# Kernel optimization log

Measured on AMD Instinct MI355X. Metric: run time of the kernel, lower is better.

The kernel has to match this reference:

```python
import jax, jax.numpy as jnp
import numpy as np

MIN_EXPERT_CAPACITY = 4
EPS = 1e-9
CAPACITY_FACTOR = 2.0  # eval capacity factor


def cumsum_exclusive(t, axis):
    return jnp.cumsum(t, axis=axis) - t


def safe_one_hot(idx, depth):
    # one_hot with an extra slot so idx == depth maps to nothing, then slice
    return jax.nn.one_hot(idx, depth + 1)[..., :depth]


def setup_inputs() -> dict:
    key = jax.random.key(0)
    k_x, k_g, k_w1, k_w2 = jax.random.split(key, 4)
    b, n, d, e, h = 2, 4096, 512, 16, 2048
    x = jax.random.normal(k_x, (b, n, d), dtype=jnp.float32)
    w_gating = jax.random.normal(k_g, (d, e), dtype=jnp.float32) / np.sqrt(d)
    w1 = jax.random.normal(k_w1, (e, d, h), dtype=jnp.float32) / np.sqrt(d)
    w2 = jax.random.normal(k_w2, (e, h, d), dtype=jnp.float32) / np.sqrt(h)
    return {"x": x, "w_gating": w_gating, "w1": w1, "w2": w2}


def top2_gating(x, w_gating):
    b, n, d = x.shape
    e = w_gating.shape[-1]
    raw_gates = jax.nn.softmax(jnp.einsum('bnd,de->bne', x, w_gating), axis=-1)

    gate_1 = jnp.max(raw_gates, axis=-1)
    index_1 = jnp.argmax(raw_gates, axis=-1)
    mask_1 = jax.nn.one_hot(index_1, e, dtype=raw_gates.dtype)

    gates_without_top1 = raw_gates * (1.0 - mask_1)
    gate_2 = jnp.max(gates_without_top1, axis=-1)
    index_2 = jnp.argmax(gates_without_top1, axis=-1)
    mask_2 = jax.nn.one_hot(index_2, e, dtype=raw_gates.dtype)

    denom = gate_1 + gate_2 + EPS
    gate_1 = gate_1 / denom
    gate_2 = gate_2 / denom

    # load-balancing loss
    density_1 = jnp.mean(mask_1, axis=-2)
    density_1_proxy = jnp.mean(raw_gates, axis=-2)
    loss = jnp.mean(density_1_proxy * density_1) * float(e * e)

    # second policy == 'all' -> keep mask_2 as-is

    capacity = max(min(n, int((n * 2) * CAPACITY_FACTOR / e)), MIN_EXPERT_CAPACITY)
    cap_f = float(capacity)

    pos1 = cumsum_exclusive(mask_1, axis=-2) * mask_1  # [b,n,e]
    mask_1 = mask_1 * (pos1 < cap_f).astype(mask_1.dtype)
    mask_1_count = jnp.sum(mask_1, axis=-2, keepdims=True)
    mask_1_flat = jnp.sum(mask_1, axis=-1)  # [b,n]
    pos1 = jnp.sum(pos1, axis=-1)
    gate_1 = gate_1 * mask_1_flat

    pos2 = (cumsum_exclusive(mask_2, axis=-2) + mask_1_count) * mask_2
    mask_2 = mask_2 * (pos2 < cap_f).astype(mask_2.dtype)
    mask_2_flat = jnp.sum(mask_2, axis=-1)
    pos2 = jnp.sum(pos2, axis=-1)
    gate_2 = gate_2 * mask_2_flat

    # combine tensor: [b, n, e, c]
    combine = (gate_1[..., None, None] * mask_1_flat[..., None, None]
               * jax.nn.one_hot(index_1, e, dtype=x.dtype)[..., None]
               * safe_one_hot(pos1.astype(jnp.int32), capacity)[..., None, :]
               + gate_2[..., None, None] * mask_2_flat[..., None, None]
               * jax.nn.one_hot(index_2, e, dtype=x.dtype)[..., None]
               * safe_one_hot(pos2.astype(jnp.int32), capacity)[..., None, :])
    dispatch = (combine > 0).astype(combine.dtype)
    return dispatch, combine, loss


def reference(x, w_gating, w1, w2):
    dispatch, combine, loss = top2_gating(x, w_gating)
    # dispatch: gather tokens into expert buckets [e, b, c, d]
    expert_inputs = jnp.einsum('bnd,bnec->ebcd', x, dispatch)
    # expert FFN (eval mode: dropout is identity)
    hidden = jax.nn.relu(jnp.einsum('ebcd,edh->ebch', expert_inputs, w1))
    expert_outputs = jnp.einsum('ebch,ehd->ebcd', hidden, w2)
    # combine back to token order, weighted by gate values
    output = jnp.einsum('ebcd,bnec->bnd', expert_outputs, combine)
    return output
```

## Files before the change

### kernel.cpp

```cpp
#include <hip/hip_runtime.h>

#define BB 2
#define NN 4096
#define DD 512
#define EE 16
#define HH 2048
#define CAP 1024
#define NTOK (BB*NN)
#define MM (BB*CAP)
#define MAXSTRIP 160

typedef unsigned short ushort_t;
typedef __attribute__((ext_vector_type(8))) short bf16x8;
typedef __attribute__((ext_vector_type(4))) float floatx4;

__device__ __forceinline__ ushort_t f2bf(float f) {
    union { float f; unsigned u; } v; v.f = f;
    unsigned r = v.u + 0x7fffu + ((v.u >> 16) & 1u);
    return (ushort_t)(r >> 16);
}

__device__ __forceinline__ void cp16(const void* g, void* l) {
    __builtin_amdgcn_global_load_lds(
        (const __attribute__((address_space(1))) void*)g,
        (__attribute__((address_space(3))) void*)l, 16, 0, 0);
}

__launch_bounds__(256)
__global__ void gating_kernel(const float* __restrict__ x,
                              const float* __restrict__ wg,
                              int* __restrict__ e1, int* __restrict__ e2,
                              float* __restrict__ g1, float* __restrict__ g2) {
    int wave = threadIdx.x >> 6;
    int lane = threadIdx.x & 63;
    int t = blockIdx.x * 4 + wave;
    const float* xp = x + (size_t)t * DD;

    float acc[EE];
#pragma unroll
    for (int e = 0; e < EE; e++) acc[e] = 0.f;
    for (int d = lane; d < DD; d += 64) {
        float xv = xp[d];
        const float* wrow = wg + d * EE;
#pragma unroll
        for (int e = 0; e < EE; e++) acc[e] = fmaf(xv, wrow[e], acc[e]);
    }
#pragma unroll
    for (int off = 32; off > 0; off >>= 1) {
#pragma unroll
        for (int e = 0; e < EE; e++) acc[e] += __shfl_xor(acc[e], off, 64);
    }
    if (lane == 0) {
        float m = acc[0];
#pragma unroll
        for (int e = 1; e < EE; e++) m = fmaxf(m, acc[e]);
        float p[EE]; float s = 0.f;
#pragma unroll
        for (int e = 0; e < EE; e++) { p[e] = __expf(acc[e] - m); s += p[e]; }
        float inv = 1.f / s;
#pragma unroll
        for (int e = 0; e < EE; e++) p[e] *= inv;
        int i1 = 0; float v1 = p[0];
#pragma unroll
        for (int e = 1; e < EE; e++) if (p[e] > v1) { v1 = p[e]; i1 = e; }
        int i2 = (i1 == 0) ? 1 : 0; float v2 = p[i2];
#pragma unroll
        for (int e = 0; e < EE; e++)
            if (e != i1 && p[e] > v2) { v2 = p[e]; i2 = e; }
        float denom = v1 + v2 + 1e-9f;
        e1[t] = i1; e2[t] = i2;
        g1[t] = v1 / denom; g2[t] = v2 / denom;
    }
}

__launch_bounds__(256)
__global__ void scan_kernel(const int* __restrict__ e1, const int* __restrict__ e2,
                            const float* __restrict__ g1, const float* __restrict__ g2,
                            int* __restrict__ s2t, float* __restrict__ s2g,
                            int* __restrict__ used) {
    int b = blockIdx.x / EE;
    int e = blockIdx.x % EE;
    int tid = threadIdx.x;
    const int base = b * NN;
    int n0 = tid * 16;

    unsigned m1 = 0, m2 = 0;
    int c1 = 0, c2 = 0;
#pragma unroll
    for (int j = 0; j < 16; j++) {
        int n = n0 + j;
        if (e1[base + n] == e) { m1 |= 1u << j; c1++; }
        if (e2[base + n] == e) { m2 |= 1u << j; c2++; }
    }
    __shared__ int s1[256], s2[256];
    s1[tid] = c1; s2[tid] = c2;
    __syncthreads();
    for (int off = 1; off < 256; off <<= 1) {
        int a1 = (tid >= off) ? s1[tid - off] : 0;
        int a2 = (tid >= off) ? s2[tid - off] : 0;
        __syncthreads();
        s1[tid] += a1; s2[tid] += a2;
        __syncthreads();
    }
    int total1 = s1[255];
    int total2 = s2[255];
    int kept1 = min(total1, CAP);
    int ex1 = s1[tid] - c1;
    int ex2 = s2[tid] - c2 + kept1;
    const int sbase = (e * BB + b) * CAP;
#pragma unroll
    for (int j = 0; j < 16; j++) {
        int n = n0 + j;
        if (m1 & (1u << j)) {
            if (ex1 < CAP) { s2t[sbase + ex1] = base + n; s2g[sbase + ex1] = g1[base + n]; }
            ex1++;
        }
        if (m2 & (1u << j)) {
            if (ex2 < CAP) { s2t[sbase + ex2] = base + n; s2g[sbase + ex2] = g2[base + n]; }
            ex2++;
        }
    }
    if (tid == 255) {
        int kept2 = min(total2, max(0, CAP - kept1));
        used[e * BB + b] = kept1 + kept2;
    }
}

__launch_bounds__(256)
__global__ void xbf_kernel(const float* __restrict__ x, ushort_t* __restrict__ xbf) {
    int i = blockIdx.x * 256 + threadIdx.x;
    float4 v = ((const float4*)x)[i];
    ushort4 h;
    h.x = f2bf(v.x); h.y = f2bf(v.y); h.z = f2bf(v.z); h.w = f2bf(v.w);
    ((ushort4*)xbf)[i] = h;
}

__global__ void worklist_kernel(const int* __restrict__ used, int* __restrict__ wl) {
    __shared__ int ns[32], pre[32];
    int i = threadIdx.x;
    if (i < 32) {
        int e = i >> 1, b = i & 1;
        ns[i] = (used[e * BB + b] + 127) >> 7;
    }
    __syncthreads();
    if (i == 0) {
        int acc = 0;
        for (int j = 0; j < 32; j++) { pre[j] = acc; acc += ns[j]; }
        wl[MAXSTRIP] = acc;
    }
    __syncthreads();
    if (i < 32) {
        int e = i >> 1, b = i & 1;
        int p = pre[i];
        for (int s = 0; s < ns[i]; s++)
            wl[p + s] = (e << 16) | (b * 8 + s);
    }
}

__global__ void transpose_bf16(const float* __restrict__ in,
                               ushort_t* __restrict__ outp, int R, int C) {
    __shared__ float tile[32][33];
    const float* slab = in + (size_t)blockIdx.z * R * C;
    ushort_t* oslab = outp + (size_t)blockIdx.z * R * C;
    int c0 = blockIdx.x * 32, r0 = blockIdx.y * 32;
    int tx = threadIdx.x, ty = threadIdx.y;
#pragma unroll
    for (int j = 0; j < 4; j++)
        tile[ty + j * 8][tx] = slab[(size_t)(r0 + ty + j * 8) * C + c0 + tx];
    __syncthreads();
#pragma unroll
    for (int j = 0; j < 4; j++)
        oslab[(size_t)(c0 + ty + j * 8) * R + r0 + tx] = f2bf(tile[tx][ty + j * 8]);
}

template <int MODE>
__launch_bounds__(256)
__global__ void gemm_mfma(const ushort_t* __restrict__ Abase,
                          const ushort_t* __restrict__ Bt,
                          void* __restrict__ Cout,
                          const int* __restrict__ wl,
                          const int* __restrict__ s2t,
                          const float* __restrict__ s2g) {
    int wi = blockIdx.y;
    if (wi >= wl[MAXSTRIP]) return;
    int entry = wl[wi];
    int e = entry >> 16;
    int ytile = entry & 0xffff;

    const int N = (MODE == 0) ? HH : DD;
    const int K = (MODE == 0) ? DD : HH;
    const int kIters = (MODE == 0) ? (DD / 32) : (HH / 2 / 32);
    int col0 = blockIdx.x * 128;
    int kOff = (MODE == 0) ? 0 : blockIdx.z * (HH / 2);

    __shared__ ushort_t As[128 * 32];
    __shared__ ushort_t Bs[128 * 32];

    int tid = threadIdx.x;
    int lane = tid & 63;
    int wid = tid >> 6;
    int wave_m = (wid & 1) << 6;
    int wave_n = (wid >> 1) << 6;
    int lm = lane & 15;
    int quad = lane >> 4;
    int sw = (quad ^ ((lm >> 1) & 3)) * 8;

    const ushort_t* aptr[2];
    const ushort_t* bptr[2];
    bool aval[2];
#pragma unroll
    for (int it = 0; it < 2; it++) {
        int idx = it * 256 + tid;
        int r = idx >> 2;
        int c = (idx & 3) ^ ((idx >> 3) & 3);
        if (MODE == 0) {
            int tok = s2t[e * MM + ytile * 128 + r];
            aval[it] = (tok >= 0);
            aptr[it] = Abase + (size_t)(tok < 0 ? 0 : tok) * DD + c * 8;
        } else {
            aval[it] = true;
            aptr[it] = Abase + (size_t)(wi * 128 + r) * HH + kOff + c * 8;
        }
        bptr[it] = Bt + (size_t)e * N * K + (size_t)(col0 + r) * K + kOff + c * 8;
    }

    floatx4 acc[4][4];
#pragma unroll
    for (int i = 0; i < 4; i++)
#pragma unroll
        for (int j = 0; j < 4; j++)
            acc[i][j] = (floatx4)(0.f);

    for (int ki = 0; ki < kIters; ki++) {
#pragma unroll
        for (int it = 0; it < 2; it++) {
            int idx = it * 256 + tid;
            if (aval[it]) cp16(aptr[it], &As[idx * 8]);
            cp16(bptr[it], &Bs[idx * 8]);
            aptr[it] += 32; bptr[it] += 32;
        }
        __syncthreads();

        bf16x8 af[4], bfr[4];
#pragma unroll
        for (int mt = 0; mt < 4; mt++)
            af[mt] = *(const bf16x8*)&As[(wave_m + mt * 16 + lm) * 32 + sw];
#pragma unroll
        for (int nt = 0; nt < 4; nt++)
            bfr[nt] = *(const bf16x8*)&Bs[(wave_n + nt * 16 + lm) * 32 + sw];
#pragma unroll
        for (int mt = 0; mt < 4; mt++)
#pragma unroll
            for (int nt = 0; nt < 4; nt++)
                acc[mt][nt] = __builtin_amdgcn_mfma_f32_16x16x32_bf16(
                    af[mt], bfr[nt], acc[mt][nt], 0, 0, 0);
        __syncthreads();
    }

    if (MODE == 0) {
        ushort_t* hp = (ushort_t*)Cout + (size_t)wi * 128 * HH;
#pragma unroll
        for (int mt = 0; mt < 4; mt++) {
#pragma unroll
            for (int r = 0; r < 4; r++) {
                int row = wave_m + mt * 16 + quad * 4 + r;
#pragma unroll
                for (int nt = 0; nt < 4; nt++) {
                    int col = col0 + wave_n + nt * 16 + lm;
                    hp[(size_t)row * HH + col] = f2bf(fmaxf(acc[mt][nt][r], 0.f));
                }
            }
        }
    } else {
        float* outp = (float*)Cout;
#pragma unroll
        for (int mt = 0; mt < 4; mt++) {
#pragma unroll
            for (int r = 0; r < 4; r++) {
                int row = wave_m + mt * 16 + quad * 4 + r;
                int slot = e * MM + ytile * 128 + row;
                int tok = s2t[slot];
                if (tok < 0) continue;
                float g = s2g[slot];
#pragma unroll
                for (int nt = 0; nt < 4; nt++) {
                    int col = col0 + wave_n + nt * 16 + lm;
                    atomicAdd(outp + (size_t)tok * DD + col, g * acc[mt][nt][r]);
                }
            }
        }
    }
}

extern "C" void kernel_launch(void* const* d_in, const int* in_sizes, int n_in,
                              void* d_out, int out_size, void* d_ws, size_t ws_size,
                              hipStream_t stream) {
    const float* x  = (const float*)d_in[0];
    const float* wg = (const float*)d_in[1];
    const float* w1 = (const float*)d_in[2];
    const float* w2 = (const float*)d_in[3];
    float* out = (float*)d_out;

    char* ws = (char*)d_ws;
    int*      e1   = (int*)(ws);
    int*      e2   = (int*)(ws + 32768);
    float*    g1   = (float*)(ws + 65536);
    float*    g2   = (float*)(ws + 98304);
    int*      used = (int*)(ws + 131072);
    int*      wl   = (int*)(ws + 132096);
    int*      s2t  = (int*)(ws + 133120);
    float*    s2g  = (float*)(ws + 264192);
    ushort_t* xbf  = (ushort_t*)(ws + 395264);
    ushort_t* wt   = (ushort_t*)(ws + 8783872);
    ushort_t* hid  = (ushort_t*)(ws + 42338304);

    hipMemsetAsync(s2t, 0xFF, 131072, stream);
    hipMemsetAsync(out, 0, (size_t)NTOK * DD * sizeof(float), stream);

    gating_kernel<<<NTOK / 4, 256, 0, stream>>>(x, wg, e1, e2, g1, g2);
    scan_kernel<<<BB * EE, 256, 0, stream>>>(e1, e2, g1, g2, s2t, s2g, used);
    xbf_kernel<<<NTOK * DD / 4 / 256, 256, 0, stream>>>(x, xbf);
    worklist_kernel<<<1, 64, 0, stream>>>(used, wl);

    transpose_bf16<<<dim3(HH / 32, DD / 32, EE), dim3(32, 8), 0, stream>>>(w1, wt, DD, HH);
    gemm_mfma<0><<<dim3(HH / 128, MAXSTRIP), 256, 0, stream>>>(xbf, wt, hid, wl, s2t, s2g);

    transpose_bf16<<<dim3(DD / 32, HH / 32, EE), dim3(32, 8), 0, stream>>>(w2, wt, HH, DD);
    gemm_mfma<1><<<dim3(DD / 128, MAXSTRIP, 2), 256, 0, stream>>>(hid, wt, out, wl, s2t, s2g);
}
```

Baseline: 378.5 us.

## Double-buffer MoE GEMMs, fuse bf16 cast into gating, retile second GEMM

The GEMM main loop now double-buffers LDS tiles and prefetches the next K-slice with raw s_waitcnt/s_barrier, so global-to-LDS loads overlap MFMA work. The x-to-bf16 conversion moves into the gating kernel, which now reads x with float4 loads, and the separate xbf kernel is removed. Resetting unused s2t slots to -1 moves from a memset into the scan kernel. The second GEMM changes from 128-wide tiles with a K-split over two z-slices to 64-wide tiles over the full K, which halves the atomicAdd traffic. All A rows are now loaded, including padded ones, and the hand-written wait counts depend on the exact number of async copies issued.

```diff
diff --git a/kernel.cpp b/kernel.cpp
--- a/kernel.cpp
+++ b/kernel.cpp
@@ -30,20 +30,32 @@
 __global__ void gating_kernel(const float* __restrict__ x,
                               const float* __restrict__ wg,
                               int* __restrict__ e1, int* __restrict__ e2,
-                              float* __restrict__ g1, float* __restrict__ g2) {
+                              float* __restrict__ g1, float* __restrict__ g2,
+                              ushort_t* __restrict__ xbf) {
     int wave = threadIdx.x >> 6;
     int lane = threadIdx.x & 63;
     int t = blockIdx.x * 4 + wave;
     const float* xp = x + (size_t)t * DD;
 
+    float4 xa = ((const float4*)xp)[lane * 2];
+    float4 xb = ((const float4*)xp)[lane * 2 + 1];
+    float xs[8] = {xa.x, xa.y, xa.z, xa.w, xb.x, xb.y, xb.z, xb.w};
+
+    ushort4 h0, h1;
+    h0.x = f2bf(xs[0]); h0.y = f2bf(xs[1]); h0.z = f2bf(xs[2]); h0.w = f2bf(xs[3]);
+    h1.x = f2bf(xs[4]); h1.y = f2bf(xs[5]); h1.z = f2bf(xs[6]); h1.w = f2bf(xs[7]);
+    ushort4* xo = (ushort4*)(xbf + (size_t)t * DD);
+    xo[lane * 2] = h0; xo[lane * 2 + 1] = h1;
+
     float acc[EE];
 #pragma unroll
     for (int e = 0; e < EE; e++) acc[e] = 0.f;
-    for (int d = lane; d < DD; d += 64) {
-        float xv = xp[d];
-        const float* wrow = wg + d * EE;
-#pragma unroll
-        for (int e = 0; e < EE; e++) acc[e] = fmaf(xv, wrow[e], acc[e]);
+    int d0 = lane * 8;
+#pragma unroll
+    for (int j = 0; j < 8; j++) {
+        const float* wrow = wg + (d0 + j) * EE;
+#pragma unroll
+        for (int e = 0; e < EE; e++) acc[e] = fmaf(xs[j], wrow[e], acc[e]);
     }
 #pragma unroll
     for (int off = 32; off > 0; off >>= 1) {
@@ -93,6 +105,7 @@
         if (e2[base + n] == e) { m2 |= 1u << j; c2++; }
     }
     __shared__ int s1[256], s2[256];
+    __shared__ int s_used;
     s1[tid] = c1; s2[tid] = c2;
     __syncthreads();
     for (int off = 1; off < 256; off <<= 1) {
@@ -122,17 +135,12 @@
     }
     if (tid == 255) {
         int kept2 = min(total2, max(0, CAP - kept1));
-        used[e * BB + b] = kept1 + kept2;
-    }
-}
-
-__launch_bounds__(256)
-__global__ void xbf_kernel(const float* __restrict__ x, ushort_t* __restrict__ xbf) {
-    int i = blockIdx.x * 256 + threadIdx.x;
-    float4 v = ((const float4*)x)[i];
-    ushort4 h;
-    h.x = f2bf(v.x); h.y = f2bf(v.y); h.z = f2bf(v.z); h.w = f2bf(v.w);
-    ((ushort4*)xbf)[i] = h;
+        int u = kept1 + kept2;
+        used[e * BB + b] = u;
+        s_used = u;
+    }
+    __syncthreads();
+    for (int i = s_used + tid; i < CAP; i += 256) s2t[sbase + i] = -1;
 }
 
 __global__ void worklist_kernel(const int* __restrict__ used, int* __restrict__ wl) {
@@ -181,86 +189,100 @@
                           const int* __restrict__ wl,
                           const int* __restrict__ s2t,
                           const float* __restrict__ s2g) {
+    constexpr int TN = (MODE == 0) ? 128 : 64;
+    constexpr int K  = (MODE == 0) ? DD : HH;
+    constexpr int KITERS = K / 32;
+    constexpr int NV = (MODE == 0) ? 4 : 3;
+    constexpr int MT = (MODE == 0) ? 4 : 2;
+
     int wi = blockIdx.y;
     if (wi >= wl[MAXSTRIP]) return;
     int entry = wl[wi];
     int e = entry >> 16;
     int ytile = entry & 0xffff;
-
-    const int N = (MODE == 0) ? HH : DD;
-    const int K = (MODE == 0) ? DD : HH;
-    const int kIters = (MODE == 0) ? (DD / 32) : (HH / 2 / 32);
-    int col0 = blockIdx.x * 128;
-    int kOff = (MODE == 0) ? 0 : blockIdx.z * (HH / 2);
-
-    __shared__ ushort_t As[128 * 32];
-    __shared__ ushort_t Bs[128 * 32];
+    int col0 = blockIdx.x * TN;
+
+    __shared__ ushort_t As[2][128 * 32];
+    __shared__ ushort_t Bs[2][TN * 32];
 
     int tid = threadIdx.x;
     int lane = tid & 63;
     int wid = tid >> 6;
-    int wave_m = (wid & 1) << 6;
-    int wave_n = (wid >> 1) << 6;
+    int wave_m = (MODE == 0) ? ((wid & 1) << 6) : (wid << 5);
+    int wave_n = (MODE == 0) ? ((wid >> 1) << 6) : 0;
     int lm = lane & 15;
     int quad = lane >> 4;
     int sw = (quad ^ ((lm >> 1) & 3)) * 8;
 
-    const ushort_t* aptr[2];
-    const ushort_t* bptr[2];
-    bool aval[2];
+    const ushort_t* ga[2];
+    const ushort_t* gb[NV - 2];
 #pragma unroll
     for (int it = 0; it < 2; it++) {
         int idx = it * 256 + tid;
         int r = idx >> 2;
-        int c = (idx & 3) ^ ((idx >> 3) & 3);
+        int cg = (idx & 3) ^ ((r >> 1) & 3);
         if (MODE == 0) {
             int tok = s2t[e * MM + ytile * 128 + r];
-            aval[it] = (tok >= 0);
-            aptr[it] = Abase + (size_t)(tok < 0 ? 0 : tok) * DD + c * 8;
+            if (tok < 0) tok = 0;
+            ga[it] = Abase + (size_t)tok * DD + cg * 8;
         } else {
-            aval[it] = true;
-            aptr[it] = Abase + (size_t)(wi * 128 + r) * HH + kOff + c * 8;
-        }
-        bptr[it] = Bt + (size_t)e * N * K + (size_t)(col0 + r) * K + kOff + c * 8;
-    }
-
-    floatx4 acc[4][4];
-#pragma unroll
-    for (int i = 0; i < 4; i++)
+            ga[it] = Abase + (size_t)(wi * 128 + r) * HH + cg * 8;
+        }
+    }
+#pragma unroll
+    for (int it = 0; it < NV - 2; it++) {
+        int idx = it * 256 + tid;
+        int r = idx >> 2;
+        int cg = (idx & 3) ^ ((r >> 1) & 3);
+        gb[it] = Bt + (size_t)e * HH * DD + (size_t)(col0 + r) * K + cg * 8;
+    }
+
+    auto stage = [&](int buf, int ki) {
+#pragma unroll
+        for (int it = 0; it < 2; it++)
+            cp16(ga[it] + ki * 32, &As[buf][(it * 256 + tid) * 8]);
+#pragma unroll
+        for (int it = 0; it < NV - 2; it++)
+            cp16(gb[it] + ki * 32, &Bs[buf][(it * 256 + tid) * 8]);
+    };
+
+    floatx4 acc[MT][4];
+#pragma unroll
+    for (int i = 0; i < MT; i++)
 #pragma unroll
         for (int j = 0; j < 4; j++)
             acc[i][j] = (floatx4)(0.f);
 
-    for (int ki = 0; ki < kIters; ki++) {
-#pragma unroll
-        for (int it = 0; it < 2; it++) {
-            int idx = it * 256 + tid;
-            if (aval[it]) cp16(aptr[it], &As[idx * 8]);
-            cp16(bptr[it], &Bs[idx * 8]);
-            aptr[it] += 32; bptr[it] += 32;
-        }
-        __syncthreads();
-
-        bf16x8 af[4], bfr[4];
-#pragma unroll
-        for (int mt = 0; mt < 4; mt++)
-            af[mt] = *(const bf16x8*)&As[(wave_m + mt * 16 + lm) * 32 + sw];
+    stage(0, 0);
+#pragma unroll 2
+    for (int ki = 0; ki < KITERS; ki++) {
+        int cur = ki & 1;
+        if (ki + 1 < KITERS) {
+            stage(cur ^ 1, ki + 1);
+            asm volatile("s_waitcnt vmcnt(%0)\ns_barrier" :: "i"(NV) : "memory");
+        } else {
+            asm volatile("s_waitcnt vmcnt(0)\ns_barrier" ::: "memory");
+        }
+        bf16x8 af[MT], bfr[4];
+#pragma unroll
+        for (int mt = 0; mt < MT; mt++)
+            af[mt] = *(const bf16x8*)&As[cur][(wave_m + mt * 16 + lm) * 32 + sw];
 #pragma unroll
         for (int nt = 0; nt < 4; nt++)
-            bfr[nt] = *(const bf16x8*)&Bs[(wave_n + nt * 16 + lm) * 32 + sw];
-#pragma unroll
-        for (int mt = 0; mt < 4; mt++)
+            bfr[nt] = *(const bf16x8*)&Bs[cur][(wave_n + nt * 16 + lm) * 32 + sw];
+#pragma unroll
+        for (int mt = 0; mt < MT; mt++)
 #pragma unroll
             for (int nt = 0; nt < 4; nt++)
                 acc[mt][nt] = __builtin_amdgcn_mfma_f32_16x16x32_bf16(
                     af[mt], bfr[nt], acc[mt][nt], 0, 0, 0);
-        __syncthreads();
+        asm volatile("s_waitcnt lgkmcnt(0)\ns_barrier" ::: "memory");
     }
 
     if (MODE == 0) {
         ushort_t* hp = (ushort_t*)Cout + (size_t)wi * 128 * HH;
 #pragma unroll
-        for (int mt = 0; mt < 4; mt++) {
+        for (int mt = 0; mt < MT; mt++) {
 #pragma unroll
             for (int r = 0; r < 4; r++) {
                 int row = wave_m + mt * 16 + quad * 4 + r;
@@ -274,7 +296,7 @@
     } else {
         float* outp = (float*)Cout;
 #pragma unroll
-        for (int mt = 0; mt < 4; mt++) {
+        for (int mt = 0; mt < MT; mt++) {
 #pragma unroll
             for (int r = 0; r < 4; r++) {
                 int row = wave_m + mt * 16 + quad * 4 + r;
@@ -314,17 +336,15 @@
     ushort_t* wt   = (ushort_t*)(ws + 8783872);
     ushort_t* hid  = (ushort_t*)(ws + 42338304);
 
-    hipMemsetAsync(s2t, 0xFF, 131072, stream);
     hipMemsetAsync(out, 0, (size_t)NTOK * DD * sizeof(float), stream);
 
-    gating_kernel<<<NTOK / 4, 256, 0, stream>>>(x, wg, e1, e2, g1, g2);
+    gating_kernel<<<NTOK / 4, 256, 0, stream>>>(x, wg, e1, e2, g1, g2, xbf);
     scan_kernel<<<BB * EE, 256, 0, stream>>>(e1, e2, g1, g2, s2t, s2g, used);
-    xbf_kernel<<<NTOK * DD / 4 / 256, 256, 0, stream>>>(x, xbf);
     worklist_kernel<<<1, 64, 0, stream>>>(used, wl);
 
     transpose_bf16<<<dim3(HH / 32, DD / 32, EE), dim3(32, 8), 0, stream>>>(w1, wt, DD, HH);
     gemm_mfma<0><<<dim3(HH / 128, MAXSTRIP), 256, 0, stream>>>(xbf, wt, hid, wl, s2t, s2g);
 
     transpose_bf16<<<dim3(DD / 32, HH / 32, EE), dim3(32, 8), 0, stream>>>(w2, wt, HH, DD);
-    gemm_mfma<1><<<dim3(DD / 128, MAXSTRIP, 2), 256, 0, stream>>>(hid, wt, out, wl, s2t, s2g);
-}
+    gemm_mfma<1><<<dim3(DD / 64, MAXSTRIP), 256, 0, stream>>>(hid, wt, out, wl, s2t, s2g);
+}
```

Result: slower. 394.4 us (+4.2%).
